# Optimization experiments

Measured on AMD Instinct MI355X. Metric: run time of the kernel, lower is better.

The kernel has to match this reference:

```python
import jax, jax.numpy as jnp
import numpy as np

K = 8            # hard-coded knn k
NS = 0.2         # LeakyReLU negative slope
EPS = 1e-6
LN_EPS = 1e-5
H = 6            # num_heads


def vn_lin(W, x):
    # VNLinear: linear over vector-channel dim (axis 1). x: (B, Cin, 3, ...)
    return jnp.einsum('oc,bc...->bo...', W, x)


def vn_leaky(x, W, U):
    # VNLinearLeakyReLU (no BN): feature map p, direction map d
    p = vn_lin(W, x)
    d = vn_lin(U, x)
    dot = jnp.sum(p * d, axis=2, keepdims=True)
    dsq = jnp.sum(d * d, axis=2, keepdims=True)
    neg = p - (dot / (dsq + EPS)) * d
    return NS * p + (1.0 - NS) * jnp.where(dot >= 0, p, neg)


def vn_layernorm(x, g, b):
    # LayerNorm on per-channel vector norms, rescale directions. x: (B,C,3,N)
    n = jnp.sqrt(jnp.sum(x * x, axis=2) + EPS)            # (B,C,N)
    mu = jnp.mean(n, axis=1, keepdims=True)
    var = jnp.var(n, axis=1, keepdims=True)
    nhat = (n - mu) / jnp.sqrt(var + LN_EPS)
    nnew = g[None, :, None] * nhat + b[None, :, None]
    return x * (nnew / n)[:, :, None, :]


def vn_attention(vn_x, Wq, Wk, Wv, Wo):
    # vn_x: (B, C, 3, N); VNLinear(C, 3C) projections, multi-head SDPA over N
    B, C, _, N = vn_x.shape
    def heads(W):
        t = vn_lin(W, vn_x)                               # (B, 3C, 3, N)
        t = t.reshape(B, H, 3 * C // H, 3, N)
        return t.transpose(0, 1, 4, 2, 3).reshape(B, H, N, -1)  # (B,H,N,9C/H)
    q, k, v = heads(Wq), heads(Wk), heads(Wv)
    scale = (3 * C // H) ** -0.5                          # head_dim = dim//H = 64
    attn = jax.nn.softmax(jnp.einsum('bhqd,bhkd->bhqk', q, k) * scale, axis=-1)
    o = jnp.einsum('bhqk,bhkd->bhqd', attn, v)            # (B,H,N,9C/H)
    o = o.transpose(0, 2, 1, 3).reshape(B, N, 3 * C, 3).transpose(0, 2, 3, 1)
    return vn_lin(Wo, o)                                  # (B, C, 3, N)


def vn_get_graph_feature(x, knn_index):
    # x: (B, C, 3, N); knn_index: flat (B*K*N,) into (B*N) rows
    B, C, _, N = x.shape
    xp = x.transpose(0, 3, 1, 2).reshape(B * N, C * 3)
    feat = xp[knn_index].reshape(B, K, N, C, 3)
    xc = x.transpose(0, 3, 1, 2).reshape(B, 1, N, C, 3)
    f = jnp.concatenate([feat - xc, jnp.broadcast_to(xc, (B, K, N, C, 3))], axis=3)
    return f.transpose(0, 3, 4, 2, 1)                     # (B, 2C, 3, N, K)


def setup_inputs() -> dict:
    key = jax.random.key(0)
    ks = jax.random.split(key, 20)
    B, N, C = 4, 2048, 128
    def w(k, o, i):
        return jax.random.normal(k, (o, i), jnp.float32) * (i ** -0.5)
    return {
        'x': jax.random.normal(ks[0], (B, N, 3 * C), jnp.float32),
        'knn_index': jax.random.randint(ks[1], (B * K * N,), 0, B * N),
        'g1': jnp.ones((C,), jnp.float32), 'b1': jnp.zeros((C,), jnp.float32),
        'g2': jnp.ones((C,), jnp.float32), 'b2': jnp.zeros((C,), jnp.float32),
        'Wq': w(ks[2], 3 * C, C), 'Wk': w(ks[3], 3 * C, C), 'Wv': w(ks[4], 3 * C, C),
        'Wo': w(ks[5], C, 3 * C),
        'W1': w(ks[6], C, 2 * C), 'U1': w(ks[7], C, 2 * C),   # conv1: 256->128
        'W2': w(ks[8], C, 2 * C),                               # conv2: 256->128
        'W3': w(ks[9], 2 * C, C), 'U3': w(ks[10], 2 * C, C),   # conv3: 128->256
        'W4': w(ks[11], C, 2 * C), 'U4': w(ks[12], C, 2 * C),  # conv4: 256->128
    }


def reference(x, knn_index, g1, b1, g2, b2, Wq, Wk, Wv, Wo, W1, U1, W2, W3, U3, W4, U4):
    B, N, D = x.shape
    C = D // 3
    vn_x = x.transpose(0, 2, 1).reshape(B, C, 3, N)
    norm_x = vn_layernorm(vn_x, g1, b1)
    x_1 = vn_attention(norm_x, Wq, Wk, Wv, Wo)            # (B,C,3,N)
    knn_f = vn_get_graph_feature(norm_x, knn_index)       # (B,2C,3,N,K)
    knn_f = vn_leaky(knn_f, W1, U1)                       # (B,C,3,N,K)
    knn_f = jnp.mean(knn_f, axis=-1)                      # mean_pool over k
    x_1 = jnp.concatenate([x_1, knn_f], axis=1)           # (B,2C,3,N)
    x_1 = vn_lin(W2, x_1)                                 # (B,C,3,N)
    vn_x = vn_x + x_1
    nx2 = vn_layernorm(vn_x, g2, b2)
    h = vn_leaky(nx2, W3, U3)                             # (B,2C,3,N)
    h = vn_leaky(h, W4, U4)                               # (B,C,3,N)
    vn_x = vn_x + h
    return vn_x.reshape(B, D, N).transpose(0, 2, 1)       # (B,N,384)
```

## Files before the change

kernel.cpp:

```cpp
#include <hip/hip_runtime.h>
#include <math.h>

#define NFIX 2048
#define HH 6
#define KNN 8
#define NSLOPE 0.2f
#define EPSF 1e-6f
#define LNEPSF 1e-5f
#define QSCALE 0.18033688011112042f
#define NSPLIT 2

typedef unsigned short ushort_t;
typedef unsigned int uint_t;
typedef __attribute__((ext_vector_type(8))) short bf16x8;
typedef __attribute__((ext_vector_type(4))) short bf16x4;
typedef __attribute__((ext_vector_type(8))) _Float16 f16x8;
typedef __attribute__((ext_vector_type(4))) _Float16 f16x4;
typedef __attribute__((ext_vector_type(16))) float f32x16;
typedef __attribute__((ext_vector_type(4))) float f32x4;

__device__ __forceinline__ ushort_t f2bf(float f) {
  union { float f; unsigned u; } v; v.f = f;
  unsigned r = v.u + 0x7fff + ((v.u >> 16) & 1);
  return (ushort_t)(r >> 16);
}
__device__ __forceinline__ float bf2f(ushort_t u) {
  union { uint_t u; float f; } v; v.u = ((uint_t)u) << 16; return v.f;
}
__device__ __forceinline__ uint_t pack2(float a, float b) {
  return (uint_t)f2bf(a) | ((uint_t)f2bf(b) << 16);
}
__device__ __forceinline__ ushort_t f2h_bits(float a) {
  union { _Float16 h; ushort_t s; } cv; cv.h = (_Float16)a; return cv.s;
}
__device__ __forceinline__ uint_t packh2(float a, float b) {
  union { _Float16 h; ushort_t s; } ha, hb;
  ha.h = (_Float16)a; hb.h = (_Float16)b;
  return (uint_t)ha.s | ((uint_t)hb.s << 16);
}

__device__ __forceinline__ void vnleaky3(const float* p, const float* dv, float* out) {
  float dot = p[0]*dv[0] + p[1]*dv[1] + p[2]*dv[2];
  float dsq = dv[0]*dv[0] + dv[1]*dv[1] + dv[2]*dv[2] + EPSF;
  float f = dot / dsq;
#pragma unroll
  for (int d = 0; d < 3; ++d) {
    float neg = p[d] - f * dv[d];
    out[d] = NSLOPE * p[d] + (1.f - NSLOPE) * ((dot >= 0.f) ? p[d] : neg);
  }
}

__global__ void prep_weights(const float* __restrict__ Wq, const float* __restrict__ Wk,
                             const float* __restrict__ Wv, const float* __restrict__ Wo,
                             const float* __restrict__ W1, const float* __restrict__ U1,
                             const float* __restrict__ W2, const float* __restrict__ W3,
                             const float* __restrict__ U3, const float* __restrict__ W4,
                             const float* __restrict__ U4,
                             ushort_t* __restrict__ Wall, _Float16* __restrict__ Af16,
                             _Float16* __restrict__ W3h, _Float16* __restrict__ U3h,
                             _Float16* __restrict__ W4h, _Float16* __restrict__ U4h) {
  int idx = blockIdx.x * 256 + threadIdx.x;
  if (idx < 212992) {
    int m = idx >> 7, c = idx & 127;
    float val;
    if (m < 384)       val = Wq[m*128 + c] * QSCALE;
    else if (m < 768)  val = Wk[(m-384)*128 + c];
    else if (m < 1152) val = Wv[(m-768)*128 + c];
    else {
      int j = m - 1152;
      if (j < 128)      val = W1[j*256 + c];
      else if (j < 256) val = U1[(j-128)*256 + c];
      else if (j < 384) { int o = j-256; val = W1[o*256 + 128 + c] - W1[o*256 + c]; }
      else              { int o = j-384; val = U1[o*256 + 128 + c] - U1[o*256 + c]; }
    }
    Wall[idx] = f2bf(val); return;
  }
  idx -= 212992;
  if (idx < 49152) {
    int j = idx / 128, c = idx % 128;
    float s = 0.f;
    for (int cp = 0; cp < 128; ++cp) s += W2[c*256 + cp] * Wo[cp*384 + j];
    Af16[(size_t)c*512 + j] = (_Float16)s; return;
  }
  idx -= 49152;
  if (idx < 16384) {
    int c2 = idx / 128, c = idx % 128;
    Af16[(size_t)c*512 + 384 + c2] = (_Float16)W2[c*256 + 128 + c2]; return;
  }
  idx -= 16384;
  if (idx < 32768) { W3h[idx] = (_Float16)W3[idx]; return; }
  idx -= 32768;
  if (idx < 32768) { U3h[idx] = (_Float16)U3[idx]; return; }
  idx -= 32768;
  if (idx < 32768) { W4h[idx] = (_Float16)W4[idx]; return; }
  idx -= 32768;
  if (idx < 32768) { U4h[idx] = (_Float16)U4[idx]; return; }
}

__global__ __launch_bounds__(128) void ln1_kernel(const float* __restrict__ in,
                                                  ushort_t* __restrict__ xbp,
                                                  float* __restrict__ xdi,
                                                  const float* __restrict__ g,
                                                  const float* __restrict__ b) {
  int bn = blockIdx.x;
  int c = threadIdx.x;
  const float* row = in + (size_t)bn * 384;
  float x0 = row[c*3+0], x1 = row[c*3+1], x2 = row[c*3+2];
  float nv = sqrtf(x0*x0 + x1*x1 + x2*x2 + EPSF);
  float s1 = nv, s2 = nv*nv;
#pragma unroll
  for (int off = 32; off >= 1; off >>= 1) {
    s1 += __shfl_down(s1, off);
    s2 += __shfl_down(s2, off);
  }
  __shared__ float red[4];
  int lane = threadIdx.x & 63, w = threadIdx.x >> 6;
  if (lane == 0) { red[w*2] = s1; red[w*2+1] = s2; }
  __syncthreads();
  float tot1 = red[0] + red[2], tot2 = red[1] + red[3];
  float mu  = tot1 * (1.f/128.f);
  float var = tot2 * (1.f/128.f) - mu*mu;
  float rsig = rsqrtf(var + LNEPSF);
  float nnew = g[c] * ((nv - mu) * rsig) + b[c];
  float sc = nnew / nv;
  size_t rb = (size_t)bn * 384;
  xbp[rb + c]       = f2bf(x0*sc);
  xbp[rb + 128 + c] = f2bf(x1*sc);
  xbp[rb + 256 + c] = f2bf(x2*sc);
  xdi[rb + c]       = x0;
  xdi[rb + 128 + c] = x1;
  xdi[rb + 256 + c] = x2;
}

#define XT_PITCH 132
#define WT_PITCH 132
#define TR_PITCH 36
__global__ __launch_bounds__(256, 2) void qkv_conv1_mfma(
    const ushort_t* __restrict__ xb, const ushort_t* __restrict__ Wall,
    ushort_t* __restrict__ q, ushort_t* __restrict__ k, ushort_t* __restrict__ v,
    _Float16* __restrict__ YZh, _Float16* __restrict__ NBh) {
  __shared__ ushort_t xs[128*XT_PITCH];
  __shared__ ushort_t wt[32*WT_PITCH];
  __shared__ float tr[4][32*TR_PITCH];
  int nb = blockIdx.x % 192;
  int mq = blockIdx.x / 192;
  int n0 = nb * 128;
  int t = threadIdx.x;
  int w = t >> 6, lane = t & 63, ql = lane & 31, hl = lane >> 5;
  for (int idx = t; idx < 2048; idx += 256) {
    int n = idx >> 4, c16 = idx & 15;
    bf16x8 gv = *(const bf16x8*)&xb[(size_t)(n0 + n)*128 + c16*8];
    ushort_t* dst = &xs[n*XT_PITCH + c16*8];
    *(bf16x4*)dst = __builtin_shufflevector(gv, gv, 0, 1, 2, 3);
    *(bf16x4*)(dst+4) = __builtin_shufflevector(gv, gv, 4, 5, 6, 7);
  }
  __syncthreads();
  bf16x8 xf[8];
  {
    const ushort_t* xr = &xs[(w*32 + ql)*XT_PITCH + hl*8];
#pragma unroll
    for (int cs = 0; cs < 8; ++cs) {
      bf16x4 lo = *(const bf16x4*)(xr + cs*16);
      bf16x4 hi = *(const bf16x4*)(xr + cs*16 + 4);
      xf[cs] = __builtin_shufflevector(lo, hi, 0, 1, 2, 3, 4, 5, 6, 7);
    }
  }
  int ng = n0 + w*32 + ql;
  int pt = ng / 3;
  int d  = ng - 3*pt;
  float* trw = tr[w];
  for (int mt = 0; mt < 13; ++mt) {
    int m0 = mq*416 + mt*32;
    __syncthreads();
    for (int idx = t; idx < 512; idx += 256) {
      int mm = idx >> 4, c16 = idx & 15;
      bf16x8 gv = *(const bf16x8*)&Wall[(size_t)(m0 + mm)*128 + c16*8];
      ushort_t* dst = &wt[mm*WT_PITCH + c16*8];
      *(bf16x4*)dst = __builtin_shufflevector(gv, gv, 0, 1, 2, 3);
      *(bf16x4*)(dst+4) = __builtin_shufflevector(gv, gv, 4, 5, 6, 7);
    }
    __syncthreads();
    f32x16 acc;
#pragma unroll
    for (int r = 0; r < 16; ++r) acc[r] = 0.f;
    const ushort_t* wr = &wt[ql*WT_PITCH + hl*8];
#pragma unroll
    for (int cs = 0; cs < 8; ++cs) {
      bf16x4 lo = *(const bf16x4*)(wr + cs*16);
      bf16x4 hi = *(const bf16x4*)(wr + cs*16 + 4);
      bf16x8 af = __builtin_shufflevector(lo, hi, 0, 1, 2, 3, 4, 5, 6, 7);
      acc = __builtin_amdgcn_mfma_f32_32x32x16_bf16(af, xf[cs], acc, 0, 0, 0);
    }
#pragma unroll
    for (int r = 0; r < 16; ++r) {
      int mrow = (r&3) + 8*(r>>2) + 4*hl;
      trw[ql*TR_PITCH + mrow] = acc[r];
    }
    asm volatile("s_waitcnt lgkmcnt(0)" ::: "memory");
    float4 c0 = *(float4*)&trw[ql*TR_PITCH + hl*16 + 0];
    float4 c1 = *(float4*)&trw[ql*TR_PITCH + hl*16 + 4];
    float4 c2 = *(float4*)&trw[ql*TR_PITCH + hl*16 + 8];
    float4 c3 = *(float4*)&trw[ql*TR_PITCH + hl*16 + 12];
    asm volatile("s_waitcnt lgkmcnt(0)" ::: "memory");
    int mg = m0 + hl*16;
    if (m0 < 1152) {
      uint4 s0, s1;
      s0.x = pack2(c0.x, c0.y); s0.y = pack2(c0.z, c0.w);
      s0.z = pack2(c1.x, c1.y); s0.w = pack2(c1.z, c1.w);
      s1.x = pack2(c2.x, c2.y); s1.y = pack2(c2.z, c2.w);
      s1.z = pack2(c3.x, c3.y); s1.w = pack2(c3.z, c3.w);
      ushort_t* dst;
      if (m0 < 384)       dst = q + (size_t)pt*1152 + d*384 + mg;
      else if (m0 < 768)  dst = k + (size_t)pt*1152 + d*384 + (mg - 384);
      else                dst = v + (size_t)pt*1152 + d*384 + (mg - 768);
      *(uint4*)dst = s0;
      *(uint4*)(dst + 8) = s1;
    } else {
      int mat = mg - 1152;
      int sub = mat >> 7, o = mat & 127;
      _Float16* basep = (sub < 2) ? YZh : NBh;
      _Float16* dst = basep + (size_t)pt*768 + d*256 + (sub & 1)*128 + o;
      uint4 s0, s1;
      s0.x = packh2(c0.x, c0.y); s0.y = packh2(c0.z, c0.w);
      s0.z = packh2(c1.x, c1.y); s0.w = packh2(c1.z, c1.w);
      s1.x = packh2(c2.x, c2.y); s1.y = packh2(c2.z, c2.w);
      s1.z = packh2(c3.x, c3.y); s1.w = packh2(c3.z, c3.w);
      *(uint4*)dst = s0;
      *(uint4*)(dst + 8) = s1;
    }
  }
}

__global__ __launch_bounds__(128) void conv1_post(const _Float16* __restrict__ YZh,
    const _Float16* __restrict__ NBh, const int* __restrict__ knn_index,
    _Float16* __restrict__ kmf16) {
  int bn = blockIdx.x;
  int b = bn / NFIX, n = bn % NFIX;
  int t = threadIdx.x;
  __shared__ int sidx[KNN];
  if (t < KNN) sidx[t] = knn_index[(b*KNN + t)*NFIX + n];
  __syncthreads();
  float yb[3], zb[3];
#pragma unroll
  for (int d = 0; d < 3; ++d) {
    yb[d] = (float)NBh[(size_t)bn*768 + d*256 + t];
    zb[d] = (float)NBh[(size_t)bn*768 + d*256 + 128 + t];
  }
  float om[3] = {0.f, 0.f, 0.f};
#pragma unroll
  for (int kk = 0; kk < KNN; ++kk) {
    const _Float16* r = YZh + (size_t)sidx[kk]*768;
    float p[3], dd[3];
#pragma unroll
    for (int d = 0; d < 3; ++d) {
      p[d]  = (float)r[d*256 + t] + yb[d];
      dd[d] = (float)r[d*256 + 128 + t] + zb[d];
    }
    float res[3];
    vnleaky3(p, dd, res);
    om[0] += res[0]; om[1] += res[1]; om[2] += res[2];
  }
#pragma unroll
  for (int d = 0; d < 3; ++d)
    kmf16[((size_t)bn*3 + d)*128 + t] = (_Float16)(om[d] * (1.f/KNN));
}

#define VT_LP 196
__global__ __launch_bounds__(256) void vtrans_kernel(const ushort_t* __restrict__ v,
                                                     ushort_t* __restrict__ vT) {
  __shared__ ushort_t tl[64*VT_LP];
  int blk = blockIdx.x;
  int bh = blk / 32, ptile = blk % 32;
  int b = bh / HH, h = bh % HH;
  int pt0 = ptile * 64;
  int t = threadIdx.x;
#pragma unroll
  for (int i = 0; i < 6; ++i) {
    int u = i*256 + t;
    int p = u / 24, seg = u % 24;
    int d = seg >> 3, c8 = seg & 7;
    bf16x8 gv = *(const bf16x8*)&v[(size_t)(b*NFIX + pt0 + p)*1152 + d*384 + h*64 + c8*8];
    ushort_t* dst = &tl[p*VT_LP + d*64 + c8*8];
    *(bf16x4*)dst = __builtin_shufflevector(gv, gv, 0, 1, 2, 3);
    *(bf16x4*)(dst+4) = __builtin_shufflevector(gv, gv, 4, 5, 6, 7);
  }
  __syncthreads();
#pragma unroll
  for (int i = 0; i < 6; ++i) {
    int u = i*256 + t;
    int ch = u >> 3, pc = u & 7;
    int ol = ch / 3, dd = ch - 3*ol;
    int cloc = dd*64 + ol;
    ushort_t hv[8];
#pragma unroll
    for (int e = 0; e < 8; ++e)
      hv[e] = tl[(pc*8 + e)*VT_LP + cloc];
    uint4 o4;
    o4.x = (uint_t)hv[0] | ((uint_t)hv[1] << 16);
    o4.y = (uint_t)hv[2] | ((uint_t)hv[3] << 16);
    o4.z = (uint_t)hv[4] | ((uint_t)hv[5] << 16);
    o4.w = (uint_t)hv[6] | ((uint_t)hv[7] << 16);
    *(uint4*)&vT[((size_t)bh*192 + ch)*2048 + pt0 + pc*8] = o4;
  }
}

#define KT_P 196
#define VT_P 36
#define TW_P 195
__global__ __launch_bounds__(256, 2) void attn_kernel(const ushort_t* __restrict__ q,
    const ushort_t* __restrict__ k, const ushort_t* __restrict__ vT,
    ushort_t* __restrict__ opart, float* __restrict__ lpart) {
  __shared__ ushort_t kt[2][32*KT_P];
  __shared__ ushort_t vt[2][192*VT_P];
  __shared__ float alds[4][32];
  int blk = blockIdx.x;
  int xcd = blk & 7, j = blk >> 3;
  int g = xcd*6 + (j >> 4);
  int qt = j & 15;
  int bh = g % 24;
  int split = g / 24;
  int b = bh / HH, h = bh % HH;
  int t = threadIdx.x;
  int w = t >> 6, lane = t & 63, ql = lane & 31, hl = lane >> 5;
  int qrow0 = qt*128 + w*32;
  const ushort_t* qpb = q + (size_t)(b*NFIX + qrow0 + ql)*1152 + h*64;
  bf16x8 qf[12];
#pragma unroll
  for (int cs = 0; cs < 12; ++cs) {
    int red0 = cs*16 + hl*8;
    int dq = red0 >> 6, ml = red0 & 63;
    qf[cs] = *(const bf16x8*)(qpb + dq*384 + ml);
  }
  const ushort_t* ksrc[3]; int kdsto[3];
  const ushort_t* vsrc[3]; int vdsto[3];
#pragma unroll
  for (int j2 = 0; j2 < 3; ++j2) {
    int idx = t + j2*256;
    int kp = idx / 24, c16 = idx % 24;
    int red0 = c16*8;
    int dk = red0 >> 6, ml = red0 & 63;
    ksrc[j2] = k + (size_t)(b*NFIX + kp)*1152 + dk*384 + h*64 + ml;
    kdsto[j2] = kp*KT_P + c16*8;
    int ch = idx >> 2, c4 = idx & 3;
    vsrc[j2] = vT + ((size_t)bh*192 + ch)*2048 + c4*8;
    vdsto[j2] = ch*VT_P + c4*8;
  }
  f32x16 acc[6];
#pragma unroll
  for (int nt = 0; nt < 6; ++nt)
#pragma unroll
    for (int r = 0; r < 16; ++r) acc[nt][r] = 0.f;
  float lsum = 0.f;
  int koff0 = split * 1024;
  bf16x8 kpre[3], vpre[3];
#pragma unroll
  for (int j2 = 0; j2 < 3; ++j2) {
    kpre[j2] = *(const bf16x8*)(ksrc[j2] + (size_t)koff0*1152);
    vpre[j2] = *(const bf16x8*)(vsrc[j2] + koff0);
  }
#pragma unroll
  for (int j2 = 0; j2 < 3; ++j2) {
    ushort_t* kd = &kt[0][kdsto[j2]];
    *(bf16x4*)kd = __builtin_shufflevector(kpre[j2], kpre[j2], 0, 1, 2, 3);
    *(bf16x4*)(kd+4) = __builtin_shufflevector(kpre[j2], kpre[j2], 4, 5, 6, 7);
    ushort_t* vd = &vt[0][vdsto[j2]];
    *(bf16x4*)vd = __builtin_shufflevector(vpre[j2], vpre[j2], 0, 1, 2, 3);
    *(bf16x4*)(vd+4) = __builtin_shufflevector(vpre[j2], vpre[j2], 4, 5, 6, 7);
  }
  __syncthreads();
  for (int kb = 0; kb < 32; ++kb) {
    int cur = kb & 1;
    if (kb < 31) {
      int koff = koff0 + (kb+1)*32;
#pragma unroll
      for (int j2 = 0; j2 < 3; ++j2) {
        kpre[j2] = *(const bf16x8*)(ksrc[j2] + (size_t)koff*1152);
        vpre[j2] = *(const bf16x8*)(vsrc[j2] + koff);
      }
    }
    f32x16 sca, scb;
#pragma unroll
    for (int r = 0; r < 16; ++r) { sca[r] = 0.f; scb[r] = 0.f; }
    const ushort_t* ktc = kt[cur];
#pragma unroll
    for (int cs = 0; cs < 12; ++cs) {
      const ushort_t* kr = &ktc[ql*KT_P + cs*16 + hl*8];
      bf16x4 alo = *(const bf16x4*)kr;
      bf16x4 ahi = *(const bf16x4*)(kr + 4);
      bf16x8 af = __builtin_shufflevector(alo, ahi, 0, 1, 2, 3, 4, 5, 6, 7);
      if (cs & 1) scb = __builtin_amdgcn_mfma_f32_32x32x16_bf16(af, qf[cs], scb, 0, 0, 0);
      else        sca = __builtin_amdgcn_mfma_f32_32x32x16_bf16(af, qf[cs], sca, 0, 0, 0);
    }
    uint_t u[8], pex[8];
#pragma unroll
    for (int g2 = 0; g2 < 4; ++g2) {
      float p0 = __builtin_amdgcn_exp2f(sca[g2*4 + 0] + scb[g2*4 + 0]);
      float p1 = __builtin_amdgcn_exp2f(sca[g2*4 + 1] + scb[g2*4 + 1]);
      float p2 = __builtin_amdgcn_exp2f(sca[g2*4 + 2] + scb[g2*4 + 2]);
      float p3 = __builtin_amdgcn_exp2f(sca[g2*4 + 3] + scb[g2*4 + 3]);
      lsum += (p0 + p1) + (p2 + p3);
      u[2*g2]   = pack2(p0, p1);
      u[2*g2+1] = pack2(p2, p3);
    }
#pragma unroll
    for (int j2 = 0; j2 < 8; ++j2) pex[j2] = (uint_t)__shfl_xor((int)u[j2], 32);
    const ushort_t* vtc = vt[cur];
#pragma unroll
    for (int s = 0; s < 2; ++s) {
      uint4 au;
      au.x = hl ? pex[4*s+2] : u[4*s+0];
      au.y = hl ? pex[4*s+3] : u[4*s+1];
      au.z = hl ? u[4*s+2]   : pex[4*s+0];
      au.w = hl ? u[4*s+3]   : pex[4*s+1];
      union { uint4 ui; bf16x8 bv; } cvt; cvt.ui = au;
      bf16x8 pa = cvt.bv;
#pragma unroll
      for (int nt = 0; nt < 6; ++nt) {
        const ushort_t* vr = &vtc[(nt*32 + ql)*VT_P + s*16 + hl*8];
        bf16x4 vlo = *(const bf16x4*)vr;
        bf16x4 vhi = *(const bf16x4*)(vr + 4);
        bf16x8 vf = __builtin_shufflevector(vlo, vhi, 0, 1, 2, 3, 4, 5, 6, 7);
        acc[nt] = __builtin_amdgcn_mfma_f32_32x32x16_bf16(pa, vf, acc[nt], 0, 0, 0);
      }
    }
    if (kb < 31) {
      int nxt = cur ^ 1;
#pragma unroll
      for (int j2 = 0; j2 < 3; ++j2) {
        ushort_t* kd = &kt[nxt][kdsto[j2]];
        *(bf16x4*)kd = __builtin_shufflevector(kpre[j2], kpre[j2], 0, 1, 2, 3);
        *(bf16x4*)(kd+4) = __builtin_shufflevector(kpre[j2], kpre[j2], 4, 5, 6, 7);
        ushort_t* vd = &vt[nxt][vdsto[j2]];
        *(bf16x4*)vd = __builtin_shufflevector(vpre[j2], vpre[j2], 0, 1, 2, 3);
        *(bf16x4*)(vd+4) = __builtin_shufflevector(vpre[j2], vpre[j2], 4, 5, 6, 7);
      }
    }
    __syncthreads();
  }
  lsum += __shfl_xor(lsum, 32);
  if (lane < 32) {
    alds[w][ql] = 1.0f / lsum;
    lpart[(size_t)split*24*NFIX + (size_t)bh*NFIX + qrow0 + ql] = lsum;
  }
  asm volatile("s_waitcnt lgkmcnt(0)" ::: "memory");
  float lv[4][4];
#pragma unroll
  for (int g2 = 0; g2 < 4; ++g2) {
    f32x4 tv = *(const f32x4*)&alds[w][8*g2 + 4*hl];
#pragma unroll
    for (int rr = 0; rr < 4; ++rr) lv[g2][rr] = tv[rr];
  }
  ushort_t* tw = (w == 0) ? kt[0] : (w == 1) ? kt[1] : (w == 2) ? vt[0] : vt[1];
#pragma unroll
  for (int nt = 0; nt < 6; ++nt) {
    int ch = nt*32 + ql;
#pragma unroll
    for (int r = 0; r < 16; ++r) {
      int qrow = (r&3) + 8*(r>>2) + 4*hl;
      tw[qrow*TW_P + ch] = f2h_bits(acc[nt][r] * lv[r>>2][r&3]);
    }
  }
  asm volatile("s_waitcnt lgkmcnt(0)" ::: "memory");
  const size_t SS = (size_t)8192*1152;
  ushort_t* opb = opart + (size_t)split*SS;
  size_t nbase = (size_t)(b*NFIX + qrow0) * 3;
#pragma unroll
  for (int i = 0; i < 12; ++i) {
    int chunk = i*64 + lane;
    int nl = chunk >> 3, jc = chunk & 7;
    int qq = nl / 3, dd = nl - 3*qq;
    ushort_t hv[8];
#pragma unroll
    for (int e = 0; e < 8; ++e)
      hv[e] = tw[qq*TW_P + (jc*8 + e)*3 + dd];
    uint4 sv;
    sv.x = (uint_t)hv[0] | ((uint_t)hv[1] << 16);
    sv.y = (uint_t)hv[2] | ((uint_t)hv[3] << 16);
    sv.z = (uint_t)hv[4] | ((uint_t)hv[5] << 16);
    sv.w = (uint_t)hv[6] | ((uint_t)hv[7] << 16);
    *(uint4*)&opb[(nbase + nl)*384 + h*64 + jc*8] = sv;
  }
}

#define AP 68
#define XLP 132
__global__ __launch_bounds__(384) void x1mid_mfma(
    const float* __restrict__ xdi, const ushort_t* __restrict__ opart,
    const float* __restrict__ lpart, const _Float16* __restrict__ kmf16,
    const _Float16* __restrict__ Af16, float* __restrict__ xmid,
    _Float16* __restrict__ nxh, const float* __restrict__ g2,
    const float* __restrict__ b2) {
  __shared__ __align__(16) char smem[50944];
  _Float16* As = (_Float16*)smem;
  _Float16* Bt = (_Float16*)(smem + 17408);
  float* wlsL  = (float*)(smem + 30464);
  float* X     = (float*)smem;
  float* stats = (float*)(smem + 50688);
  int blk = blockIdx.x;
  int n0 = blk * 96;
  int pt0 = blk * 32;
  int t = threadIdx.x;
  int w = t >> 6, lane = t & 63, ql = lane & 31, hl = lane >> 5;
  int nsub = w >> 1, mh = w & 1;
  if (t < 192) {
    int ptl = t / 6, h = t % 6;
    int ptg = pt0 + ptl;
    int b = ptg >> 11, n = ptg & 2047;
    size_t lidx = (size_t)(b*HH + h)*NFIX + n;
    float l[NSPLIT]; float tot = 0.f;
#pragma unroll
    for (int s = 0; s < NSPLIT; ++s) {
      l[s] = lpart[(size_t)s*24*NFIX + lidx];
      tot += l[s];
    }
    float rd = 1.f / tot;
    float* wp = &wlsL[(ptl*6 + h)*NSPLIT];
#pragma unroll
    for (int s = 0; s < NSPLIT; ++s) wp[s] = l[s]*rd;
  }
  f32x16 acc[2];
#pragma unroll
  for (int m2 = 0; m2 < 2; ++m2)
#pragma unroll
    for (int r = 0; r < 16; ++r) acc[m2][r] = 0.f;
  const size_t SS = (size_t)8192*1152;
  __syncthreads();
  for (int p = 0; p < 8; ++p) {
    for (int u = t; u < 1024; u += 384) {
      int m = u >> 3, kc = u & 7;
      f16x4 a0 = *(const f16x4*)&Af16[(size_t)m*512 + p*64 + kc*8];
      f16x4 a1 = *(const f16x4*)&Af16[(size_t)m*512 + p*64 + kc*8 + 4];
      _Float16* dst = &As[m*AP + kc*8];
      *(f16x4*)dst = a0;
      *(f16x4*)(dst+4) = a1;
    }
    {
      int u = t;
      if (u < 384) {
        int n_l = u >> 2, jc = u & 3;
        int n_g = n0 + n_l;
        _Float16* dst = &Bt[n_l*AP + jc*16];
        if (p < 6) {
          int pt_l = n_l / 3;
          const float* wp = &wlsL[(pt_l*6 + p)*NSPLIT];
          float facc[16];
#pragma unroll
          for (int e = 0; e < 16; ++e) facc[e] = 0.f;
#pragma unroll
          for (int s = 0; s < NSPLIT; ++s) {
            const ushort_t* src = opart + s*SS + (size_t)n_g*384 + p*64 + jc*16;
            uint4 ra = *(const uint4*)src;
            uint4 rb = *(const uint4*)(src + 8);
            const _Float16* ua = (const _Float16*)&ra;
            const _Float16* ub = (const _Float16*)&rb;
            float wsc = wp[s];
#pragma unroll
            for (int e = 0; e < 8; ++e) {
              facc[e]     += wsc * (float)ua[e];
              facc[8 + e] += wsc * (float)ub[e];
            }
          }
          _Float16 hv[16];
#pragma unroll
          for (int e = 0; e < 16; ++e) hv[e] = (_Float16)facc[e];
#pragma unroll
          for (int g = 0; g < 4; ++g)
            *(f16x4*)(dst + g*4) = *(f16x4*)&hv[g*4];
        } else {
          const _Float16* src = kmf16 + (size_t)n_g*128 + (p-6)*64 + jc*16;
          f16x4 v0 = *(const f16x4*)src;
          f16x4 v1 = *(const f16x4*)(src + 4);
          f16x4 v2 = *(const f16x4*)(src + 8);
          f16x4 v3 = *(const f16x4*)(src + 12);
          *(f16x4*)dst = v0; *(f16x4*)(dst+4) = v1;
          *(f16x4*)(dst+8) = v2; *(f16x4*)(dst+12) = v3;
        }
      }
    }
    __syncthreads();
#pragma unroll
    for (int cs = 0; cs < 4; ++cs) {
      int kloc = cs*16 + hl*8;
      f16x4 b0 = *(const f16x4*)&Bt[(nsub*32 + ql)*AP + kloc];
      f16x4 b1 = *(const f16x4*)&Bt[(nsub*32 + ql)*AP + kloc + 4];
      f16x8 bf = __builtin_shufflevector(b0, b1, 0, 1, 2, 3, 4, 5, 6, 7);
#pragma unroll
      for (int m2 = 0; m2 < 2; ++m2) {
        int mrow = (mh*2 + m2)*32 + ql;
        f16x4 a0 = *(const f16x4*)&As[mrow*AP + kloc];
        f16x4 a1 = *(const f16x4*)&As[mrow*AP + kloc + 4];
        f16x8 af = __builtin_shufflevector(a0, a1, 0, 1, 2, 3, 4, 5, 6, 7);
        acc[m2] = __builtin_amdgcn_mfma_f32_32x32x16_f16(af, bf, acc[m2], 0, 0, 0);
      }
    }
    __syncthreads();
  }
#pragma unroll
  for (int m2 = 0; m2 < 2; ++m2) {
    int cbase = (mh*2 + m2)*32 + 4*hl;
    float* xrow = &X[(nsub*32 + ql)*XLP];
#pragma unroll
    for (int r = 0; r < 16; ++r) {
      int col = cbase + (r&3) + 8*(r>>2);
      xrow[col] = acc[m2][r];
    }
  }
  __syncthreads();
#pragma unroll
  for (int i = 0; i < 4; ++i) {
    int u = i*384 + t;
    int row = u >> 4, c0 = (u & 15) * 8;
    float* xp = &X[row*XLP + c0];
    const float* xd = xdi + (size_t)(n0 + row)*128 + c0;
    float4 a0 = *(float4*)xp, a1 = *(float4*)(xp + 4);
    float4 d0 = *(const float4*)xd, d1 = *(const float4*)(xd + 4);
    a0.x += d0.x; a0.y += d0.y; a0.z += d0.z; a0.w += d0.w;
    a1.x += d1.x; a1.y += d1.y; a1.z += d1.z; a1.w += d1.w;
    *(float4*)xp = a0; *(float4*)(xp + 4) = a1;
    float* dst = xmid + (size_t)(n0 + row)*128 + c0;
    *(float4*)dst = a0; *(float4*)(dst + 4) = a1;
  }
  __syncthreads();
  for (int pi = w; pi < 32; pi += 6) {
    int c = lane;
    float a0 = X[(pi*3+0)*XLP + c], a1 = X[(pi*3+1)*XLP + c], a2 = X[(pi*3+2)*XLP + c];
    float e0 = X[(pi*3+0)*XLP + c + 64], e1 = X[(pi*3+1)*XLP + c + 64], e2 = X[(pi*3+2)*XLP + c + 64];
    float nva = sqrtf(a0*a0 + a1*a1 + a2*a2 + EPSF);
    float nvb = sqrtf(e0*e0 + e1*e1 + e2*e2 + EPSF);
    float s1 = nva + nvb;
    float s2 = nva*nva + nvb*nvb;
#pragma unroll
    for (int off = 32; off >= 1; off >>= 1) {
      s1 += __shfl_down(s1, off);
      s2 += __shfl_down(s2, off);
    }
    if (lane == 0) {
      float mu = s1 * (1.f/128.f);
      float var = s2 * (1.f/128.f) - mu*mu;
      stats[pi*2]   = mu;
      stats[pi*2+1] = rsqrtf(var + LNEPSF);
    }
  }
  __syncthreads();
#pragma unroll
  for (int i = 0; i < 4; ++i) {
    int u = i*384 + t;
    int row = u >> 4, c0 = (u & 15) * 8;
    int pt_l = row / 3;
    float mu = stats[pt_l*2], rsig = stats[pt_l*2+1];
    const float* r0 = &X[(pt_l*3 + 0)*XLP + c0];
    const float* r1 = &X[(pt_l*3 + 1)*XLP + c0];
    const float* r2 = &X[(pt_l*3 + 2)*XLP + c0];
    const float* rd = &X[row*XLP + c0];
    float xv[8];
#pragma unroll
    for (int e = 0; e < 8; ++e) {
      float x0 = r0[e], x1 = r1[e], x2 = r2[e];
      float nv = sqrtf(x0*x0 + x1*x1 + x2*x2 + EPSF);
      float nnew = g2[c0 + e] * ((nv - mu) * rsig) + b2[c0 + e];
      xv[e] = rd[e] * (nnew / nv);
    }
    uint4 sv;
    sv.x = packh2(xv[0], xv[1]); sv.y = packh2(xv[2], xv[3]);
    sv.z = packh2(xv[4], xv[5]); sv.w = packh2(xv[6], xv[7]);
    *(uint4*)&nxh[(size_t)(n0 + row)*128 + c0] = sv;
  }
}

#define X3P 132
#define TR3P 36
__global__ __launch_bounds__(256) void conv3_mfma(const _Float16* __restrict__ nxh,
    const _Float16* __restrict__ W3h, const _Float16* __restrict__ U3h,
    _Float16* __restrict__ h3) {
  __shared__ __align__(16) _Float16 Xs[3*32*X3P];
  __shared__ __align__(16) _Float16 tr3[4][96*TR3P];
  int blk = blockIdx.x;
  int pt0 = (blk >> 1) * 32;
  int oh = blk & 1;
  int t = threadIdx.x;
  int w = t >> 6, lane = t & 63, ql = lane & 31, hl = lane >> 5;
#pragma unroll
  for (int i = 0; i < 6; ++i) {
    int u = i*256 + t;
    int r = u >> 4, c8 = u & 15;
    f16x8 gv = *(const f16x8*)&nxh[(size_t)(pt0*3 + r)*128 + c8*8];
    int d = r % 3, p = r / 3;
    _Float16* dst = &Xs[(d*32 + p)*X3P + c8*8];
    *(f16x4*)dst = __builtin_shufflevector(gv, gv, 0, 1, 2, 3);
    *(f16x4*)(dst+4) = __builtin_shufflevector(gv, gv, 4, 5, 6, 7);
  }
  __syncthreads();
  int ot = oh*128 + w*32;
  const _Float16* Wp = W3h + (size_t)(ot + ql)*128 + hl*8;
  const _Float16* Up = U3h + (size_t)(ot + ql)*128 + hl*8;
  f32x16 accP[3], accD[3];
#pragma unroll
  for (int d = 0; d < 3; ++d)
#pragma unroll
    for (int r = 0; r < 16; ++r) { accP[d][r] = 0.f; accD[d][r] = 0.f; }
#pragma unroll
  for (int cs = 0; cs < 8; ++cs) {
    f16x8 wf = *(const f16x8*)(Wp + cs*16);
    f16x8 uf = *(const f16x8*)(Up + cs*16);
#pragma unroll
    for (int d = 0; d < 3; ++d) {
      const _Float16* xr = &Xs[(d*32 + ql)*X3P + cs*16 + hl*8];
      f16x4 lo = *(const f16x4*)xr;
      f16x4 hi = *(const f16x4*)(xr + 4);
      f16x8 xf = __builtin_shufflevector(lo, hi, 0, 1, 2, 3, 4, 5, 6, 7);
      accP[d] = __builtin_amdgcn_mfma_f32_32x32x16_f16(wf, xf, accP[d], 0, 0, 0);
      accD[d] = __builtin_amdgcn_mfma_f32_32x32x16_f16(uf, xf, accD[d], 0, 0, 0);
    }
  }
  _Float16* trw = tr3[w];
#pragma unroll
  for (int r = 0; r < 16; ++r) {
    int olr = (r&3) + 8*(r>>2) + 4*hl;
    float p3[3], d3[3], res[3];
#pragma unroll
    for (int d = 0; d < 3; ++d) { p3[d] = accP[d][r]; d3[d] = accD[d][r]; }
    vnleaky3(p3, d3, res);
#pragma unroll
    for (int d = 0; d < 3; ++d) trw[(ql*3 + d)*TR3P + olr] = (_Float16)res[d];
  }
  asm volatile("s_waitcnt lgkmcnt(0)" ::: "memory");
#pragma unroll
  for (int i = 0; i < 6; ++i) {
    int u = i*64 + lane;
    int row = u >> 2, c8 = u & 3;
    const _Float16* src = &trw[row*TR3P + c8*8];
    f16x4 lo = *(const f16x4*)src;
    f16x4 hi = *(const f16x4*)(src + 4);
    f16x8 ov = __builtin_shufflevector(lo, hi, 0, 1, 2, 3, 4, 5, 6, 7);
    *(f16x8*)&h3[(size_t)(pt0*3 + row)*256 + ot + c8*8] = ov;
  }
}

#define X4P 260
#define TF4P 388
__global__ __launch_bounds__(256) void conv4_mfma(const _Float16* __restrict__ h3,
    const _Float16* __restrict__ W4h, const _Float16* __restrict__ U4h,
    const float* __restrict__ xmid, float* __restrict__ out) {
  __shared__ __align__(16) _Float16 Xs[3*16*X4P];
  __shared__ __align__(16) float trF[16*TF4P];
  int pt0 = blockIdx.x * 16;
  int t = threadIdx.x;
  int w = t >> 6, lane = t & 63;
  int nl = lane & 15, kq = lane >> 4;
#pragma unroll
  for (int i = 0; i < 6; ++i) {
    int u = i*256 + t;
    int r = u >> 5, c8 = u & 31;
    f16x8 gv = *(const f16x8*)&h3[(size_t)(pt0*3 + r)*256 + c8*8];
    int d = r % 3, p = r / 3;
    _Float16* dst = &Xs[(d*16 + p)*X4P + c8*8];
    *(f16x4*)dst = __builtin_shufflevector(gv, gv, 0, 1, 2, 3);
    *(f16x4*)(dst+4) = __builtin_shufflevector(gv, gv, 4, 5, 6, 7);
  }
  __syncthreads();
  int ot = w*32;
  f32x4 accP[2][3], accD[2][3];
#pragma unroll
  for (int mt = 0; mt < 2; ++mt)
#pragma unroll
    for (int d = 0; d < 3; ++d)
#pragma unroll
      for (int r = 0; r < 4; ++r) { accP[mt][d][r] = 0.f; accD[mt][d][r] = 0.f; }
  const _Float16* Wb = W4h + (size_t)ot*256;
  const _Float16* Ub = U4h + (size_t)ot*256;
#pragma unroll
  for (int cs = 0; cs < 8; ++cs) {
    int kof = cs*32 + kq*8;
    f16x8 xf[3];
#pragma unroll
    for (int d = 0; d < 3; ++d) {
      const _Float16* xr = &Xs[(d*16 + nl)*X4P + kof];
      f16x4 lo = *(const f16x4*)xr;
      f16x4 hi = *(const f16x4*)(xr + 4);
      xf[d] = __builtin_shufflevector(lo, hi, 0, 1, 2, 3, 4, 5, 6, 7);
    }
#pragma unroll
    for (int mt = 0; mt < 2; ++mt) {
      f16x8 wf = *(const f16x8*)(Wb + (size_t)(mt*16 + nl)*256 + kof);
      f16x8 uf = *(const f16x8*)(Ub + (size_t)(mt*16 + nl)*256 + kof);
#pragma unroll
      for (int d = 0; d < 3; ++d) {
        accP[mt][d] = __builtin_amdgcn_mfma_f32_16x16x32_f16(wf, xf[d], accP[mt][d], 0, 0, 0);
        accD[mt][d] = __builtin_amdgcn_mfma_f32_16x16x32_f16(uf, xf[d], accD[mt][d], 0, 0, 0);
      }
    }
  }
#pragma unroll
  for (int mt = 0; mt < 2; ++mt)
#pragma unroll
    for (int r = 0; r < 4; ++r) {
      int o = ot + mt*16 + kq*4 + r;
      float p3[3], d3[3], res[3];
#pragma unroll
      for (int d = 0; d < 3; ++d) { p3[d] = accP[mt][d][r]; d3[d] = accD[mt][d][r]; }
      vnleaky3(p3, d3, res);
#pragma unroll
      for (int d = 0; d < 3; ++d) trF[nl*TF4P + o*3 + d] = res[d];
    }
  __syncthreads();
#pragma unroll
  for (int i = 0; i < 6; ++i) {
    int u = i*256 + t;
    int row = u / 96, c4 = u % 96;
    float4 vv = *(float4*)&trF[row*TF4P + c4*4];
    int bn = pt0 + row;
    float rs[4];
    const float* fv = (const float*)&vv;
#pragma unroll
    for (int e = 0; e < 4; ++e) {
      int col = c4*4 + e;
      int o = col / 3, d = col - 3*o;
      rs[e] = fv[e] + xmid[(size_t)(3*bn + d)*128 + o];
    }
    float4 ov; ov.x = rs[0]; ov.y = rs[1]; ov.z = rs[2]; ov.w = rs[3];
    *(float4*)&out[(size_t)bn*384 + c4*4] = ov;
  }
}

extern "C" void kernel_launch(void* const* d_in, const int* in_sizes, int n_in,
                              void* d_out, int out_size, void* d_ws, size_t ws_size,
                              hipStream_t stream) {
  const float* x   = (const float*)d_in[0];
  const int* knn   = (const int*)d_in[1];
  const float* g1  = (const float*)d_in[2];
  const float* b1  = (const float*)d_in[3];
  const float* g2  = (const float*)d_in[4];
  const float* b2  = (const float*)d_in[5];
  const float* Wq  = (const float*)d_in[6];
  const float* Wk  = (const float*)d_in[7];
  const float* Wv  = (const float*)d_in[8];
  const float* Wo  = (const float*)d_in[9];
  const float* W1  = (const float*)d_in[10];
  const float* U1  = (const float*)d_in[11];
  const float* W2  = (const float*)d_in[12];
  const float* W3  = (const float*)d_in[13];
  const float* U3  = (const float*)d_in[14];
  const float* W4  = (const float*)d_in[15];
  const float* U4  = (const float*)d_in[16];
  float* out = (float*)d_out;
  (void)n_in; (void)out_size; (void)ws_size;

  const size_t BN = (size_t)in_sizes[0] / 384;

  float* ws    = (float*)d_ws;
  float* xdi   = ws;
  float* xmid  = xdi + BN*384;
  _Float16* kmf16 = (_Float16*)(xmid + BN*384);
  ushort_t* xbp = (ushort_t*)(kmf16 + BN*384);
  ushort_t* qb = xbp + BN*384;
  ushort_t* kb = qb + BN*1152;
  ushort_t* vb = kb + BN*1152;
  ushort_t* vT = vb + BN*1152;
  ushort_t* Wall = vT + BN*1152;
  _Float16* Af16 = (_Float16*)(Wall + 212992);
  _Float16* W3h = Af16 + 65536;
  _Float16* U3h = W3h + 32768;
  _Float16* W4h = U3h + 32768;
  _Float16* U4h = W4h + 32768;
  ushort_t* opart = (ushort_t*)(U4h + 32768);
  float* lpart = (float*)(opart + 4*BN*1152);
  _Float16* YZh = (_Float16*)opart;
  _Float16* NBh = YZh + BN*768;
  _Float16* nxh = (_Float16*)qb;
  _Float16* h3  = (_Float16*)kb;

  prep_weights<<<1600, 256, 0, stream>>>(Wq, Wk, Wv, Wo, W1, U1, W2, W3, U3, W4, U4,
                                         Wall, Af16, W3h, U3h, W4h, U4h);
  ln1_kernel<<<(int)BN, 128, 0, stream>>>(x, xbp, xdi, g1, b1);
  qkv_conv1_mfma<<<192*4, 256, 0, stream>>>(xbp, Wall, qb, kb, vb, YZh, NBh);
  conv1_post<<<(int)BN, 128, 0, stream>>>(YZh, NBh, knn, kmf16);
  vtrans_kernel<<<768, 256, 0, stream>>>(vb, vT);
  attn_kernel<<<16*24*NSPLIT, 256, 0, stream>>>(qb, kb, vT, opart, lpart);
  x1mid_mfma<<<256, 384, 0, stream>>>(xdi, opart, lpart, kmf16, Af16, xmid, nxh, g2, b2);
  conv3_mfma<<<512, 256, 0, stream>>>(nxh, W3h, U3h, h3);
  conv4_mfma<<<512, 256, 0, stream>>>(h3, W4h, U4h, xmid, out);
}
```

Baseline: 329.3 us.

## Deepen attention K/V prefetch to two tiles and raise MFMA priority

Restructures the attention main loop into a two-iteration unrolled macro body with two register sets of prefetched K/V tiles, so global loads for tile kb+2 are issued while tile kb is being computed. Shared-memory writes for the next tile move ahead of the softmax/PV phase, and s_setprio raises wave priority around the MFMA blocks. The QK accumulation now uses a single chained accumulator instead of two interleaved ones, which lengthens the MFMA dependency chain. The extra prefetch registers raise register pressure under launch_bounds(256,2) and may cause spills.

```diff
diff --git a/kernel.cpp b/kernel.cpp
--- a/kernel.cpp
+++ b/kernel.cpp
@@ -307,6 +307,71 @@
 #define KT_P 196
 #define VT_P 36
 #define TW_P 195
+
+#define ATTN_BODY(KB, CUR, KPW, VPW, KPL, VPL, DO_WRITE, DO_LOAD) {               \
+    f32x16 sc;                                                                     \
+    _Pragma("unroll") for (int r = 0; r < 16; ++r) sc[r] = 0.f;                    \
+    const ushort_t* ktc = kt[CUR];                                                 \
+    __builtin_amdgcn_s_setprio(1);                                                 \
+    _Pragma("unroll") for (int cs = 0; cs < 12; ++cs) {                            \
+      const ushort_t* kr = &ktc[ql*KT_P + cs*16 + hl*8];                           \
+      bf16x4 alo = *(const bf16x4*)kr;                                             \
+      bf16x4 ahi = *(const bf16x4*)(kr + 4);                                       \
+      bf16x8 af = __builtin_shufflevector(alo, ahi, 0, 1, 2, 3, 4, 5, 6, 7);       \
+      sc = __builtin_amdgcn_mfma_f32_32x32x16_bf16(af, qf[cs], sc, 0, 0, 0);       \
+    }                                                                              \
+    __builtin_amdgcn_s_setprio(0);                                                 \
+    if (DO_WRITE) {                                                                \
+      _Pragma("unroll") for (int j2 = 0; j2 < 3; ++j2) {                           \
+        ushort_t* kd = &kt[(CUR)^1][kdsto[j2]];                                    \
+        *(bf16x4*)kd = __builtin_shufflevector(KPW[j2], KPW[j2], 0, 1, 2, 3);      \
+        *(bf16x4*)(kd+4) = __builtin_shufflevector(KPW[j2], KPW[j2], 4, 5, 6, 7);  \
+        ushort_t* vd = &vt[(CUR)^1][vdsto[j2]];                                    \
+        *(bf16x4*)vd = __builtin_shufflevector(VPW[j2], VPW[j2], 0, 1, 2, 3);      \
+        *(bf16x4*)(vd+4) = __builtin_shufflevector(VPW[j2], VPW[j2], 4, 5, 6, 7);  \
+      }                                                                            \
+    }                                                                              \
+    if (DO_LOAD) {                                                                 \
+      int koff = koff0 + ((KB)+2)*32;                                              \
+      _Pragma("unroll") for (int j2 = 0; j2 < 3; ++j2) {                           \
+        KPL[j2] = *(const bf16x8*)(ksrc[j2] + (size_t)koff*1152);                  \
+        VPL[j2] = *(const bf16x8*)(vsrc[j2] + koff);                               \
+      }                                                                            \
+    }                                                                              \
+    uint_t u[8], pex[8];                                                           \
+    _Pragma("unroll") for (int g2 = 0; g2 < 4; ++g2) {                             \
+      float p0 = __builtin_amdgcn_exp2f(sc[g2*4 + 0]);                             \
+      float p1 = __builtin_amdgcn_exp2f(sc[g2*4 + 1]);                             \
+      float p2 = __builtin_amdgcn_exp2f(sc[g2*4 + 2]);                             \
+      float p3 = __builtin_amdgcn_exp2f(sc[g2*4 + 3]);                             \
+      lsum += (p0 + p1) + (p2 + p3);                                               \
+      u[2*g2]   = pack2(p0, p1);                                                   \
+      u[2*g2+1] = pack2(p2, p3);                                                   \
+    }                                                                              \
+    _Pragma("unroll") for (int j2 = 0; j2 < 8; ++j2)                               \
+      pex[j2] = (uint_t)__shfl_xor((int)u[j2], 32);                                \
+    const ushort_t* vtc = vt[CUR];                                                 \
+    __builtin_amdgcn_s_setprio(1);                                                 \
+    _Pragma("unroll") for (int s = 0; s < 2; ++s) {                                \
+      uint4 au;                                                                    \
+      au.x = hl ? pex[4*s+2] : u[4*s+0];                                           \
+      au.y = hl ? pex[4*s+3] : u[4*s+1];                                           \
+      au.z = hl ? u[4*s+2]   : pex[4*s+0];                                         \
+      au.w = hl ? u[4*s+3]   : pex[4*s+1];                                         \
+      union { uint4 ui; bf16x8 bv; } cvt_; cvt_.ui = au;                           \
+      bf16x8 pa = cvt_.bv;                                                         \
+      _Pragma("unroll") for (int nt = 0; nt < 6; ++nt) {                           \
+        const ushort_t* vr = &vtc[(nt*32 + ql)*VT_P + s*16 + hl*8];                \
+        bf16x4 vlo = *(const bf16x4*)vr;                                           \
+        bf16x4 vhi = *(const bf16x4*)(vr + 4);                                     \
+        bf16x8 vf = __builtin_shufflevector(vlo, vhi, 0, 1, 2, 3, 4, 5, 6, 7);     \
+        acc[nt] = __builtin_amdgcn_mfma_f32_32x32x16_bf16(pa, vf, acc[nt], 0, 0, 0); \
+      }                                                                            \
+    }                                                                              \
+    __builtin_amdgcn_s_setprio(0);                                                 \
+    __syncthreads();                                                               \
+  }
+
 __global__ __launch_bounds__(256, 2) void attn_kernel(const ushort_t* __restrict__ q,
     const ushort_t* __restrict__ k, const ushort_t* __restrict__ vT,
     ushort_t* __restrict__ opart, float* __restrict__ lpart) {
@@ -352,90 +417,28 @@
     for (int r = 0; r < 16; ++r) acc[nt][r] = 0.f;
   float lsum = 0.f;
   int koff0 = split * 1024;
-  bf16x8 kpre[3], vpre[3];
+  bf16x8 kpA[3], vpA[3], kpB[3], vpB[3];
 #pragma unroll
   for (int j2 = 0; j2 < 3; ++j2) {
-    kpre[j2] = *(const bf16x8*)(ksrc[j2] + (size_t)koff0*1152);
-    vpre[j2] = *(const bf16x8*)(vsrc[j2] + koff0);
+    kpA[j2] = *(const bf16x8*)(ksrc[j2] + (size_t)koff0*1152);
+    vpA[j2] = *(const bf16x8*)(vsrc[j2] + koff0);
+    kpB[j2] = *(const bf16x8*)(ksrc[j2] + (size_t)(koff0 + 32)*1152);
+    vpB[j2] = *(const bf16x8*)(vsrc[j2] + (koff0 + 32));
   }
 #pragma unroll
   for (int j2 = 0; j2 < 3; ++j2) {
     ushort_t* kd = &kt[0][kdsto[j2]];
-    *(bf16x4*)kd = __builtin_shufflevector(kpre[j2], kpre[j2], 0, 1, 2, 3);
-    *(bf16x4*)(kd+4) = __builtin_shufflevector(kpre[j2], kpre[j2], 4, 5, 6, 7);
+    *(bf16x4*)kd = __builtin_shufflevector(kpA[j2], kpA[j2], 0, 1, 2, 3);
+    *(bf16x4*)(kd+4) = __builtin_shufflevector(kpA[j2], kpA[j2], 4, 5, 6, 7);
     ushort_t* vd = &vt[0][vdsto[j2]];
-    *(bf16x4*)vd = __builtin_shufflevector(vpre[j2], vpre[j2], 0, 1, 2, 3);
-    *(bf16x4*)(vd+4) = __builtin_shufflevector(vpre[j2], vpre[j2], 4, 5, 6, 7);
-  }
-  __syncthreads();
-  for (int kb = 0; kb < 32; ++kb) {
-    int cur = kb & 1;
-    if (kb < 31) {
-      int koff = koff0 + (kb+1)*32;
-#pragma unroll
-      for (int j2 = 0; j2 < 3; ++j2) {
-        kpre[j2] = *(const bf16x8*)(ksrc[j2] + (size_t)koff*1152);
-        vpre[j2] = *(const bf16x8*)(vsrc[j2] + koff);
-      }
-    }
-    f32x16 sca, scb;
-#pragma unroll
-    for (int r = 0; r < 16; ++r) { sca[r] = 0.f; scb[r] = 0.f; }
-    const ushort_t* ktc = kt[cur];
-#pragma unroll
-    for (int cs = 0; cs < 12; ++cs) {
-      const ushort_t* kr = &ktc[ql*KT_P + cs*16 + hl*8];
-      bf16x4 alo = *(const bf16x4*)kr;
-      bf16x4 ahi = *(const bf16x4*)(kr + 4);
-      bf16x8 af = __builtin_shufflevector(alo, ahi, 0, 1, 2, 3, 4, 5, 6, 7);
-      if (cs & 1) scb = __builtin_amdgcn_mfma_f32_32x32x16_bf16(af, qf[cs], scb, 0, 0, 0);
-      else        sca = __builtin_amdgcn_mfma_f32_32x32x16_bf16(af, qf[cs], sca, 0, 0, 0);
-    }
-    uint_t u[8], pex[8];
-#pragma unroll
-    for (int g2 = 0; g2 < 4; ++g2) {
-      float p0 = __builtin_amdgcn_exp2f(sca[g2*4 + 0] + scb[g2*4 + 0]);
-      float p1 = __builtin_amdgcn_exp2f(sca[g2*4 + 1] + scb[g2*4 + 1]);
-      float p2 = __builtin_amdgcn_exp2f(sca[g2*4 + 2] + scb[g2*4 + 2]);
-      float p3 = __builtin_amdgcn_exp2f(sca[g2*4 + 3] + scb[g2*4 + 3]);
-      lsum += (p0 + p1) + (p2 + p3);
-      u[2*g2]   = pack2(p0, p1);
-      u[2*g2+1] = pack2(p2, p3);
-    }
-#pragma unroll
-    for (int j2 = 0; j2 < 8; ++j2) pex[j2] = (uint_t)__shfl_xor((int)u[j2], 32);
-    const ushort_t* vtc = vt[cur];
-#pragma unroll
-    for (int s = 0; s < 2; ++s) {
-      uint4 au;
-      au.x = hl ? pex[4*s+2] : u[4*s+0];
-      au.y = hl ? pex[4*s+3] : u[4*s+1];
-      au.z = hl ? u[4*s+2]   : pex[4*s+0];
-      au.w = hl ? u[4*s+3]   : pex[4*s+1];
-      union { uint4 ui; bf16x8 bv; } cvt; cvt.ui = au;
-      bf16x8 pa = cvt.bv;
-#pragma unroll
-      for (int nt = 0; nt < 6; ++nt) {
-        const ushort_t* vr = &vtc[(nt*32 + ql)*VT_P + s*16 + hl*8];
-        bf16x4 vlo = *(const bf16x4*)vr;
-        bf16x4 vhi = *(const bf16x4*)(vr + 4);
-        bf16x8 vf = __builtin_shufflevector(vlo, vhi, 0, 1, 2, 3, 4, 5, 6, 7);
-        acc[nt] = __builtin_amdgcn_mfma_f32_32x32x16_bf16(pa, vf, acc[nt], 0, 0, 0);
-      }
-    }
-    if (kb < 31) {
-      int nxt = cur ^ 1;
-#pragma unroll
-      for (int j2 = 0; j2 < 3; ++j2) {
-        ushort_t* kd = &kt[nxt][kdsto[j2]];
-        *(bf16x4*)kd = __builtin_shufflevector(kpre[j2], kpre[j2], 0, 1, 2, 3);
-        *(bf16x4*)(kd+4) = __builtin_shufflevector(kpre[j2], kpre[j2], 4, 5, 6, 7);
-        ushort_t* vd = &vt[nxt][vdsto[j2]];
-        *(bf16x4*)vd = __builtin_shufflevector(vpre[j2], vpre[j2], 0, 1, 2, 3);
-        *(bf16x4*)(vd+4) = __builtin_shufflevector(vpre[j2], vpre[j2], 4, 5, 6, 7);
-      }
-    }
-    __syncthreads();
+    *(bf16x4*)vd = __builtin_shufflevector(vpA[j2], vpA[j2], 0, 1, 2, 3);
+    *(bf16x4*)(vd+4) = __builtin_shufflevector(vpA[j2], vpA[j2], 4, 5, 6, 7);
+  }
+  __syncthreads();
+  for (int it = 0; it < 16; ++it) {
+    int kb0 = it*2;
+    ATTN_BODY(kb0,     0, kpB, vpB, kpA, vpA, 1,         (it < 15))
+    ATTN_BODY(kb0 + 1, 1, kpA, vpA, kpB, vpB, (it < 15), (it < 15))
   }
   lsum += __shfl_xor(lsum, 32);
   if (lane < 32) {
```

New measurement: 335.9 us. +2.0%, slower.

## Load V fragments directly from global memory instead of staging through LDS

Applied to the files above, without the earlier changes.

The attention kernel stops staging V tiles in shared memory: each wave loads its V MFMA operands straight from global/L2 into registers every key block, and the old V LDS buffers are replaced by a smaller epilogue scratch buffer. It also merges the two alternating score accumulators into one MFMA chain. This is meant to remove LDS write/read traffic and bank pressure for V. In exchange, each of the four waves now fetches the same V data separately, which adds L2 traffic, exposes global latency inside the loop without prefetch, raises register use, and the single accumulator serialises the QK MFMA dependency chain.

```diff
diff --git a/kernel.cpp b/kernel.cpp
--- a/kernel.cpp
+++ b/kernel.cpp
@@ -305,13 +305,12 @@
 }
 
 #define KT_P 196
-#define VT_P 36
 #define TW_P 195
 __global__ __launch_bounds__(256, 2) void attn_kernel(const ushort_t* __restrict__ q,
     const ushort_t* __restrict__ k, const ushort_t* __restrict__ vT,
     ushort_t* __restrict__ opart, float* __restrict__ lpart) {
   __shared__ ushort_t kt[2][32*KT_P];
-  __shared__ ushort_t vt[2][192*VT_P];
+  __shared__ ushort_t ep[2][32*KT_P];
   __shared__ float alds[4][32];
   int blk = blockIdx.x;
   int xcd = blk & 7, j = blk >> 3;
@@ -332,7 +331,6 @@
     qf[cs] = *(const bf16x8*)(qpb + dq*384 + ml);
   }
   const ushort_t* ksrc[3]; int kdsto[3];
-  const ushort_t* vsrc[3]; int vdsto[3];
 #pragma unroll
   for (int j2 = 0; j2 < 3; ++j2) {
     int idx = t + j2*256;
@@ -341,31 +339,24 @@
     int dk = red0 >> 6, ml = red0 & 63;
     ksrc[j2] = k + (size_t)(b*NFIX + kp)*1152 + dk*384 + h*64 + ml;
     kdsto[j2] = kp*KT_P + c16*8;
-    int ch = idx >> 2, c4 = idx & 3;
-    vsrc[j2] = vT + ((size_t)bh*192 + ch)*2048 + c4*8;
-    vdsto[j2] = ch*VT_P + c4*8;
-  }
+  }
+  int koff0 = split * 1024;
+  const ushort_t* vgb = vT + ((size_t)bh*192 + ql)*2048 + koff0 + hl*8;
   f32x16 acc[6];
 #pragma unroll
   for (int nt = 0; nt < 6; ++nt)
 #pragma unroll
     for (int r = 0; r < 16; ++r) acc[nt][r] = 0.f;
   float lsum = 0.f;
-  int koff0 = split * 1024;
-  bf16x8 kpre[3], vpre[3];
-#pragma unroll
-  for (int j2 = 0; j2 < 3; ++j2) {
+  bf16x8 kpre[3];
+#pragma unroll
+  for (int j2 = 0; j2 < 3; ++j2)
     kpre[j2] = *(const bf16x8*)(ksrc[j2] + (size_t)koff0*1152);
-    vpre[j2] = *(const bf16x8*)(vsrc[j2] + koff0);
-  }
 #pragma unroll
   for (int j2 = 0; j2 < 3; ++j2) {
     ushort_t* kd = &kt[0][kdsto[j2]];
     *(bf16x4*)kd = __builtin_shufflevector(kpre[j2], kpre[j2], 0, 1, 2, 3);
     *(bf16x4*)(kd+4) = __builtin_shufflevector(kpre[j2], kpre[j2], 4, 5, 6, 7);
-    ushort_t* vd = &vt[0][vdsto[j2]];
-    *(bf16x4*)vd = __builtin_shufflevector(vpre[j2], vpre[j2], 0, 1, 2, 3);
-    *(bf16x4*)(vd+4) = __builtin_shufflevector(vpre[j2], vpre[j2], 4, 5, 6, 7);
   }
   __syncthreads();
   for (int kb = 0; kb < 32; ++kb) {
@@ -373,14 +364,12 @@
     if (kb < 31) {
       int koff = koff0 + (kb+1)*32;
 #pragma unroll
-      for (int j2 = 0; j2 < 3; ++j2) {
+      for (int j2 = 0; j2 < 3; ++j2)
         kpre[j2] = *(const bf16x8*)(ksrc[j2] + (size_t)koff*1152);
-        vpre[j2] = *(const bf16x8*)(vsrc[j2] + koff);
-      }
-    }
-    f32x16 sca, scb;
-#pragma unroll
-    for (int r = 0; r < 16; ++r) { sca[r] = 0.f; scb[r] = 0.f; }
+    }
+    f32x16 sc;
+#pragma unroll
+    for (int r = 0; r < 16; ++r) sc[r] = 0.f;
     const ushort_t* ktc = kt[cur];
 #pragma unroll
     for (int cs = 0; cs < 12; ++cs) {
@@ -388,23 +377,28 @@
       bf16x4 alo = *(const bf16x4*)kr;
       bf16x4 ahi = *(const bf16x4*)(kr + 4);
       bf16x8 af = __builtin_shufflevector(alo, ahi, 0, 1, 2, 3, 4, 5, 6, 7);
-      if (cs & 1) scb = __builtin_amdgcn_mfma_f32_32x32x16_bf16(af, qf[cs], scb, 0, 0, 0);
-      else        sca = __builtin_amdgcn_mfma_f32_32x32x16_bf16(af, qf[cs], sca, 0, 0, 0);
+      sc = __builtin_amdgcn_mfma_f32_32x32x16_bf16(af, qf[cs], sc, 0, 0, 0);
+    }
+    bf16x8 vfr[12];
+#pragma unroll
+    for (int nt = 0; nt < 6; ++nt) {
+#pragma unroll
+      for (int s = 0; s < 2; ++s)
+        vfr[nt*2+s] = *(const bf16x8*)(vgb + (size_t)nt*32*2048 + kb*32 + s*16);
     }
     uint_t u[8], pex[8];
 #pragma unroll
     for (int g2 = 0; g2 < 4; ++g2) {
-      float p0 = __builtin_amdgcn_exp2f(sca[g2*4 + 0] + scb[g2*4 + 0]);
-      float p1 = __builtin_amdgcn_exp2f(sca[g2*4 + 1] + scb[g2*4 + 1]);
-      float p2 = __builtin_amdgcn_exp2f(sca[g2*4 + 2] + scb[g2*4 + 2]);
-      float p3 = __builtin_amdgcn_exp2f(sca[g2*4 + 3] + scb[g2*4 + 3]);
+      float p0 = __builtin_amdgcn_exp2f(sc[g2*4 + 0]);
+      float p1 = __builtin_amdgcn_exp2f(sc[g2*4 + 1]);
+      float p2 = __builtin_amdgcn_exp2f(sc[g2*4 + 2]);
+      float p3 = __builtin_amdgcn_exp2f(sc[g2*4 + 3]);
       lsum += (p0 + p1) + (p2 + p3);
       u[2*g2]   = pack2(p0, p1);
       u[2*g2+1] = pack2(p2, p3);
     }
 #pragma unroll
     for (int j2 = 0; j2 < 8; ++j2) pex[j2] = (uint_t)__shfl_xor((int)u[j2], 32);
-    const ushort_t* vtc = vt[cur];
 #pragma unroll
     for (int s = 0; s < 2; ++s) {
       uint4 au;
@@ -415,13 +409,8 @@
       union { uint4 ui; bf16x8 bv; } cvt; cvt.ui = au;
       bf16x8 pa = cvt.bv;
 #pragma unroll
-      for (int nt = 0; nt < 6; ++nt) {
-        const ushort_t* vr = &vtc[(nt*32 + ql)*VT_P + s*16 + hl*8];
-        bf16x4 vlo = *(const bf16x4*)vr;
-        bf16x4 vhi = *(const bf16x4*)(vr + 4);
-        bf16x8 vf = __builtin_shufflevector(vlo, vhi, 0, 1, 2, 3, 4, 5, 6, 7);
-        acc[nt] = __builtin_amdgcn_mfma_f32_32x32x16_bf16(pa, vf, acc[nt], 0, 0, 0);
-      }
+      for (int nt = 0; nt < 6; ++nt)
+        acc[nt] = __builtin_amdgcn_mfma_f32_32x32x16_bf16(pa, vfr[nt*2+s], acc[nt], 0, 0, 0);
     }
     if (kb < 31) {
       int nxt = cur ^ 1;
@@ -430,9 +419,6 @@
         ushort_t* kd = &kt[nxt][kdsto[j2]];
         *(bf16x4*)kd = __builtin_shufflevector(kpre[j2], kpre[j2], 0, 1, 2, 3);
         *(bf16x4*)(kd+4) = __builtin_shufflevector(kpre[j2], kpre[j2], 4, 5, 6, 7);
-        ushort_t* vd = &vt[nxt][vdsto[j2]];
-        *(bf16x4*)vd = __builtin_shufflevector(vpre[j2], vpre[j2], 0, 1, 2, 3);
-        *(bf16x4*)(vd+4) = __builtin_shufflevector(vpre[j2], vpre[j2], 4, 5, 6, 7);
       }
     }
     __syncthreads();
@@ -450,7 +436,7 @@
 #pragma unroll
     for (int rr = 0; rr < 4; ++rr) lv[g2][rr] = tv[rr];
   }
-  ushort_t* tw = (w == 0) ? kt[0] : (w == 1) ? kt[1] : (w == 2) ? vt[0] : vt[1];
+  ushort_t* tw = (w == 0) ? kt[0] : (w == 1) ? kt[1] : (w == 2) ? ep[0] : ep[1];
 #pragma unroll
   for (int nt = 0; nt < 6; ++nt) {
     int ch = nt*32 + ql;
```

After: 395.7 us. 1.2x slower.
